# Kernel tuning notes

Hardware: AMD Instinct MI355X
Metric: run time of the kernel (lower is better)

## Reference

```python
import jax, jax.numpy as jnp
import numpy as np

FM = 256          # feature_maps
ROUNDS = 32
N_VARS = 4000
N_CLAUSES = 16800 # ~4.2 * n_vars (3-SAT phase transition)
K = 3             # literals per clause
EPS = 1e-8


def setup_inputs() -> dict:
    key = jax.random.key(0)
    ks = jax.random.split(key, 20)

    def nrm(k, shape):
        # tf.initializers.RandomNormal default stddev = 0.05
        return jax.random.normal(k, shape, jnp.float32) * 0.05

    vs = jax.random.randint(ks[0], (N_CLAUSES, K), 1, N_VARS + 1)
    sg = jnp.where(jax.random.uniform(ks[1], (N_CLAUSES, K)) < 0.5, -1, 1)
    return {
        "clause_lits": (vs * sg).astype(jnp.int32),  # signed 1-based literals
        "n_vars": N_VARS,
        "L_init": nrm(ks[2], (1, FM)), "C_init": nrm(ks[3], (1, FM)),
        "LC_W0": nrm(ks[4], (FM, FM)), "LC_b0": jnp.zeros((FM,), jnp.float32),
        "LC_W1": nrm(ks[5], (FM, FM)), "LC_b1": jnp.zeros((FM,), jnp.float32),
        "LC_W2": nrm(ks[6], (FM, FM)), "LC_b2": jnp.zeros((FM,), jnp.float32),
        "CL_W0": nrm(ks[7], (FM, FM)), "CL_b0": jnp.zeros((FM,), jnp.float32),
        "CL_W1": nrm(ks[8], (FM, FM)), "CL_b1": jnp.zeros((FM,), jnp.float32),
        "CL_W2": nrm(ks[9], (FM, FM)), "CL_b2": jnp.zeros((FM,), jnp.float32),
        "C_Wx": nrm(ks[10], (FM, 4 * FM)), "C_Wh": nrm(ks[11], (FM, 4 * FM)),
        "C_b": jnp.zeros((4 * FM,), jnp.float32),
        "L_Wx": nrm(ks[12], (2 * FM, 4 * FM)), "L_Wh": nrm(ks[13], (FM, 4 * FM)),
        "L_b": jnp.zeros((4 * FM,), jnp.float32),
        "V_W0": nrm(ks[14], (2 * FM, 2 * FM)), "V_b0": jnp.zeros((2 * FM,), jnp.float32),
        "V_W1": nrm(ks[15], (2 * FM, 2 * FM)), "V_b1": jnp.zeros((2 * FM,), jnp.float32),
        "V_W2": nrm(ks[16], (2 * FM, 1)), "V_b2": jnp.zeros((1,), jnp.float32),
    }


def _mlp3(x, W0, b0, W1, b1, W2, b2):
    h = jax.nn.relu(x @ W0 + b0)
    h = jax.nn.relu(h @ W1 + b1)
    return h @ W2 + b2


def _lstm(x, h, c, Wx, Wh, b):
    # keras LSTMCell: gate order i, f, g, o; sigmoid recurrent, tanh activation
    z = x @ Wx + h @ Wh + b
    i, f, g, o = jnp.split(z, 4, axis=1)
    c = jax.nn.sigmoid(f) * c + jax.nn.sigmoid(i) * jnp.tanh(g)
    h = jax.nn.sigmoid(o) * jnp.tanh(c)
    return h, c


def reference(clause_lits, n_vars, L_init, C_init,
              LC_W0, LC_b0, LC_W1, LC_b1, LC_W2, LC_b2,
              CL_W0, CL_b0, CL_W1, CL_b1, CL_W2, CL_b2,
              C_Wx, C_Wh, C_b, L_Wx, L_Wh, L_b,
              V_W0, V_b0, V_W1, V_b1, V_W2, V_b2):
    n_clauses = clause_lits.shape[0]
    n_lits = 2 * n_vars
    lits = clause_lits.reshape(-1)                         # [E]
    sign = jnp.sign(lits).astype(jnp.float32)              # [E]
    var_idx = jnp.abs(lits) - 1                            # [E] 0-based var
    lit_idx = jnp.where(lits > 0, var_idx, n_vars + var_idx)
    clause_idx = jnp.repeat(jnp.arange(n_clauses), clause_lits.shape[1])

    denom = jnp.sqrt(jnp.float32(FM))
    l_h = jnp.tile(L_init / denom, (n_lits, 1))
    c_h = jnp.tile(C_init / denom, (n_clauses, 1))
    l_c = jnp.zeros_like(l_h)
    c_c = jnp.zeros_like(c_h)

    def vote(lh):
        variables = jnp.concatenate([lh[:n_vars], lh[n_vars:]], axis=1)  # [n_vars, 2*FM]
        return _mlp3(variables, V_W0, V_b0, V_W1, V_b1, V_W2, V_b2)      # [n_vars, 1]

    def clause_loss(logits):
        # softplus_log_square_loss: clause_val = exp(-sum_lit softplus(sign*logit))
        vals = logits[var_idx, 0] * sign                   # [E]
        s = jax.ops.segment_sum(jax.nn.softplus(vals), clause_idx,
                                num_segments=n_clauses, indices_are_sorted=True)
        cv = jnp.exp(-s)
        return jnp.sum(jnp.square(-jnp.log(1.0 - cv + EPS)))

    def round_fn(carry, _):
        lh, lc, ch, cc, loss = carry
        lc_pre = _mlp3(lh, LC_W0, LC_b0, LC_W1, LC_b1, LC_W2, LC_b2)
        # SpMM adj^T @ msgs: scatter literal messages into clauses
        lc_msgs = jax.ops.segment_sum(lc_pre[lit_idx], clause_idx,
                                      num_segments=n_clauses, indices_are_sorted=True)
        ch, cc = _lstm(lc_msgs, ch, cc, C_Wx, C_Wh, C_b)
        cl_pre = _mlp3(ch, CL_W0, CL_b0, CL_W1, CL_b1, CL_W2, CL_b2)
        # SpMM adj @ msgs: scatter clause messages into literals
        cl_msgs = jax.ops.segment_sum(cl_pre[clause_idx], lit_idx, num_segments=n_lits)
        flipped = jnp.concatenate([lh[n_vars:], lh[:n_vars]], axis=0)
        lh, lc = _lstm(jnp.concatenate([cl_msgs, flipped], axis=1), lh, lc,
                       L_Wx, L_Wh, L_b)
        loss = loss + clause_loss(vote(lh))
        return (lh, lc, ch, cc, loss), None

    (l_h, l_c, c_h, c_c, loss), _ = jax.lax.scan(
        round_fn, (l_h, l_c, c_h, c_c, jnp.float32(0.0)), None, length=ROUNDS)
    logits = vote(l_h)
    return logits, loss / jnp.float32(ROUNDS)
```

## Files before the change

### kernel.cpp

```cpp
#include <hip/hip_runtime.h>
#include <hip/hip_bf16.h>

#define NV 4000
#define NL 8000
#define NC 16800
#define NE 50400
#define FM 256
#define ROUNDS 32

typedef short s16x8 __attribute__((ext_vector_type(8)));
typedef __bf16 b16x8 __attribute__((ext_vector_type(8)));
typedef float f32x4 __attribute__((ext_vector_type(4)));
union V8 { s16x8 s; b16x8 b; ushort u[8]; };

using gaddr_t = const void __attribute__((address_space(1)))*;
using laddr_t = void __attribute__((address_space(3)))*;

__device__ __forceinline__ float b2f(ushort u) {
    union { uint i; float f; } v; v.i = ((uint)u) << 16; return v.f;
}
__device__ __forceinline__ ushort f2b(float f) {
    __hip_bfloat16 h = __float2bfloat16(f);
    return *(ushort*)&h;
}

__global__ void zero_kernel(float* __restrict__ p, int n) {
    int i = blockIdx.x * blockDim.x + threadIdx.x;
    if (i < n) p[i] = 0.0f;
}
__global__ void f2b_kernel(const float* __restrict__ src, ushort* __restrict__ dst, int n) {
    int i = blockIdx.x * blockDim.x + threadIdx.x;
    if (i < n) dst[i] = f2b(src[i]);
}
__global__ void transpose_w_kernel(const float* __restrict__ in, ushort* __restrict__ out,
                                   int K, int N, int ldo, int koff, int perm) {
    int idx = blockIdx.x * blockDim.x + threadIdx.x;
    if (idx >= K * N) return;
    int n = idx / K, k = idx - n * K;
    int row = perm ? ((n & 255) * 4 + (n >> 8)) : n;
    out[(size_t)row * ldo + koff + k] = f2b(in[(size_t)k * N + n]);
}
__global__ void permute_bias_kernel(const float* __restrict__ b, float* __restrict__ bp) {
    int n = blockIdx.x * blockDim.x + threadIdx.x;
    if (n < 1024) bp[(n & 255) * 4 + (n >> 8)] = b[n];
}

__global__ void init_lh_kernel(const float* __restrict__ Li, ushort* __restrict__ lh) {
    int idx = blockIdx.x * blockDim.x + threadIdx.x;
    if (idx < NL * FM) lh[idx] = f2b(Li[idx & (FM - 1)] * (1.0f / 16.0f));
}
__global__ void init_ch_kernel(const float* __restrict__ Ci, ushort* __restrict__ ch) {
    int idx = blockIdx.x * blockDim.x + threadIdx.x;
    if (idx < NC * FM) ch[idx] = f2b(Ci[idx & (FM - 1)] * (1.0f / 16.0f));
}

__global__ void csr_count_kernel(const int* __restrict__ lits, int* __restrict__ deg) {
    int e = blockIdx.x * blockDim.x + threadIdx.x;
    if (e >= NE) return;
    int l = lits[e];
    int v = (l > 0 ? l : -l) - 1;
    int li = (l > 0) ? v : NV + v;
    atomicAdd(&deg[li], 1);
}
__global__ void csr_scan_kernel(const int* __restrict__ deg, int* __restrict__ rowptr,
                                int* __restrict__ nxt) {
    if (threadIdx.x == 0 && blockIdx.x == 0) {
        int acc = 0;
        for (int i = 0; i < NL; ++i) { rowptr[i] = acc; nxt[i] = acc; acc += deg[i]; }
        rowptr[NL] = acc;
    }
}
__global__ void csr_fill_kernel(const int* __restrict__ lits, int* __restrict__ nxt,
                                int* __restrict__ ecl) {
    int e = blockIdx.x * blockDim.x + threadIdx.x;
    if (e >= NE) return;
    int l = lits[e];
    int v = (l > 0 ? l : -l) - 1;
    int li = (l > 0) ? v : NV + v;
    int pos = atomicAdd(&nxt[li], 1);
    ecl[pos] = e / 3;
}

#define BKT 64

#define MLPR 32
__global__ __launch_bounds__(256) void mlp3_kernel(
    const ushort* __restrict__ A,
    const ushort* __restrict__ W0t, const float* __restrict__ b0,
    const ushort* __restrict__ W1t, const float* __restrict__ b1,
    const ushort* __restrict__ W2t, const float* __restrict__ b2,
    ushort* __restrict__ out, int M)
{
    __shared__ __align__(16) ushort As[MLPR * BKT];
    __shared__ __align__(16) ushort Wl[256 * BKT];
    __shared__ __align__(16) ushort Ab[MLPR * 264];
    const int tid = threadIdx.x;
    const int lane = tid & 63, wid = tid >> 6;
    const int rowBase = blockIdx.x * MLPR;
    const int lr = lane >> 3, ql = (lane & 7) ^ lr;
    const int cl16 = lane & 15, kg = lane >> 4;

    const ushort* Wt[3] = {W0t, W1t, W2t};
    const float*  bs[3] = {b0, b1, b2};

    #pragma unroll
    for (int layer = 0; layer < 3; ++layer) {
        f32x4 acc[2][4];
        #pragma unroll
        for (int i = 0; i < 2; ++i)
            #pragma unroll
            for (int j = 0; j < 4; ++j) acc[i][j] = (f32x4){0.f, 0.f, 0.f, 0.f};

        for (int kt = 0; kt < 4; ++kt) {
            __syncthreads();
            #pragma unroll
            for (int t = 0; t < 8; ++t) {
                int row = wid * 64 + t * 8 + lr;
                __builtin_amdgcn_global_load_lds(
                    (gaddr_t)(Wt[layer] + (size_t)row * 256 + kt * 64 + ql * 8),
                    (laddr_t)&Wl[(wid * 64 + t * 8) * BKT + lane * 8], 16, 0, 0);
            }
            if (layer == 0) {
                int row = rowBase + wid * 8 + lr;
                if (row > M - 1) row = M - 1;
                __builtin_amdgcn_global_load_lds(
                    (gaddr_t)(A + (size_t)row * 256 + kt * 64 + ql * 8),
                    (laddr_t)&As[wid * 512 + lane * 8], 16, 0, 0);
            }
            __syncthreads();
            #pragma unroll
            for (int s = 0; s < 2; ++s) {
                int kq8 = s * 4 + kg;
                V8 af[2], bf[4];
                #pragma unroll
                for (int i = 0; i < 2; ++i) {
                    int m = i * 16 + cl16;
                    if (layer == 0)
                        af[i].s = *(const s16x8*)&As[m * BKT + ((kq8 ^ (m & 7)) * 8)];
                    else
                        af[i].s = *(const s16x8*)&Ab[m * 264 + kt * 64 + kq8 * 8];
                }
                #pragma unroll
                for (int j = 0; j < 4; ++j) {
                    int n = wid * 64 + j * 16 + cl16;
                    bf[j].s = *(const s16x8*)&Wl[n * BKT + ((kq8 ^ (n & 7)) * 8)];
                }
                #pragma unroll
                for (int i = 0; i < 2; ++i)
                    #pragma unroll
                    for (int j = 0; j < 4; ++j)
                        acc[i][j] = __builtin_amdgcn_mfma_f32_16x16x32_bf16(
                            af[i].b, bf[j].b, acc[i][j], 0, 0, 0);
            }
        }
        __syncthreads();
        const int rq = (lane >> 4) * 4;
        #pragma unroll
        for (int i = 0; i < 2; ++i)
            #pragma unroll
            for (int r = 0; r < 4; ++r) {
                int row = i * 16 + rq + r;
                #pragma unroll
                for (int j = 0; j < 4; ++j) {
                    int col = wid * 64 + j * 16 + cl16;
                    float v = acc[i][j][r] + bs[layer][col];
                    if (layer < 2) {
                        Ab[row * 264 + col] = f2b(fmaxf(v, 0.0f));
                    } else {
                        int grow = rowBase + row;
                        if (grow < M) out[(size_t)grow * 256 + col] = f2b(v);
                    }
                }
            }
    }
}

__global__ __launch_bounds__(256) void gemm16_n64_kernel(
    const ushort* __restrict__ A0, int K0,
    const ushort* __restrict__ A1, int K1,
    const ushort* __restrict__ Bt, const float* __restrict__ bias,
    ushort* __restrict__ C, int M, int N, int relu)
{
    __shared__ __align__(16) ushort Al[128 * BKT];
    __shared__ __align__(16) ushort Bl[64 * BKT];
    const int Ktot = K0 + K1;
    const int tid = threadIdx.x;
    const int rowBase = blockIdx.y * 128, colBase = blockIdx.x * 64;
    const int lane = tid & 63, wid = tid >> 6;
    const int wm = (wid & 1) * 64, wn = (wid >> 1) * 32;
    const int lr = lane >> 3, ql = (lane & 7) ^ lr;

    f32x4 acc[4][2];
    #pragma unroll
    for (int i = 0; i < 4; ++i)
        #pragma unroll
        for (int j = 0; j < 2; ++j) acc[i][j] = (f32x4){0.f, 0.f, 0.f, 0.f};

    for (int k0 = 0; k0 < Ktot; k0 += BKT) {
        const ushort* As; int ks, lda;
        if (k0 < K0) { As = A0; ks = k0; lda = K0; }
        else         { As = A1; ks = k0 - K0; lda = K1; }
        __syncthreads();
        #pragma unroll
        for (int t = 0; t < 4; ++t) {
            int rloc = (wid * 4 + t) * 8 + lr;
            int ga = rowBase + rloc; if (ga > M - 1) ga = M - 1;
            __builtin_amdgcn_global_load_lds((gaddr_t)(As + (size_t)ga * lda + ks + ql * 8),
                                             (laddr_t)&Al[(wid * 4 + t) * 512], 16, 0, 0);
        }
        #pragma unroll
        for (int t = 0; t < 2; ++t) {
            int rloc = (wid * 2 + t) * 8 + lr;
            __builtin_amdgcn_global_load_lds((gaddr_t)(Bt + (size_t)(colBase + rloc) * Ktot + k0 + ql * 8),
                                             (laddr_t)&Bl[(wid * 2 + t) * 512], 16, 0, 0);
        }
        __syncthreads();
        const int cl = lane & 15, kg = lane >> 4;
        #pragma unroll
        for (int s = 0; s < 2; ++s) {
            V8 af[4], bf[2];
            #pragma unroll
            for (int i = 0; i < 4; ++i) {
                int m = wm + i * 16 + cl;
                af[i].s = *(const s16x8*)&Al[m * BKT + (((s * 4 + kg) ^ (m & 7)) * 8)];
            }
            #pragma unroll
            for (int j = 0; j < 2; ++j) {
                int n = wn + j * 16 + cl;
                bf[j].s = *(const s16x8*)&Bl[n * BKT + (((s * 4 + kg) ^ (n & 7)) * 8)];
            }
            #pragma unroll
            for (int i = 0; i < 4; ++i)
                #pragma unroll
                for (int j = 0; j < 2; ++j)
                    acc[i][j] = __builtin_amdgcn_mfma_f32_16x16x32_bf16(af[i].b, bf[j].b,
                                                                        acc[i][j], 0, 0, 0);
        }
    }
    const int rq = (lane >> 4) * 4, cl = lane & 15;
    #pragma unroll
    for (int i = 0; i < 4; ++i)
        #pragma unroll
        for (int r = 0; r < 4; ++r) {
            int grow = rowBase + wm + i * 16 + rq + r;
            if (grow >= M) continue;
            #pragma unroll
            for (int j = 0; j < 2; ++j) {
                int gcol = colBase + wn + j * 16 + cl;
                float v = acc[i][j][r] + bias[gcol];
                if (relu) v = fmaxf(v, 0.0f);
                C[(size_t)grow * N + gcol] = f2b(v);
            }
        }
}

__global__ __launch_bounds__(256) void gemm_lstm_kernel(
    const ushort* __restrict__ A0, int K0,
    const ushort* __restrict__ A1, int K1,
    const ushort* __restrict__ A2, int K2,
    int flip1,
    const ushort* __restrict__ Bt, const float* __restrict__ biasP,
    float* __restrict__ c32, ushort* __restrict__ h_out, int M)
{
    __shared__ __align__(16) ushort smem[2 * 128 * BKT];
    ushort* Al = smem;
    ushort* Bl = smem + 128 * BKT;
    const int Ktot = K0 + K1 + K2;
    const int tid = threadIdx.x;
    const int rowBase = blockIdx.y * 128, colBase = blockIdx.x * 128;
    const int lane = tid & 63, wid = tid >> 6;
    const int wm = (wid >> 1) * 64, wn = (wid & 1) * 64;
    const int lr = lane >> 3, ql = (lane & 7) ^ lr;

    f32x4 acc[4][4];
    #pragma unroll
    for (int i = 0; i < 4; ++i)
        #pragma unroll
        for (int j = 0; j < 4; ++j) acc[i][j] = (f32x4){0.f, 0.f, 0.f, 0.f};

    for (int k0 = 0; k0 < Ktot; k0 += BKT) {
        const ushort* As; int ks, lda, flip;
        if (k0 < K0)           { As = A0; ks = k0;           lda = K0; flip = 0; }
        else if (k0 < K0 + K1) { As = A1; ks = k0 - K0;      lda = K1; flip = flip1; }
        else                   { As = A2; ks = k0 - K0 - K1; lda = K2; flip = 0; }
        __syncthreads();
        #pragma unroll
        for (int t = 0; t < 4; ++t) {
            int rloc = (wid * 4 + t) * 8 + lr;
            int ga = rowBase + rloc; if (ga > M - 1) ga = M - 1;
            if (flip) ga = (ga < NV) ? ga + NV : ga - NV;
            __builtin_amdgcn_global_load_lds((gaddr_t)(As + (size_t)ga * lda + ks + ql * 8),
                                             (laddr_t)&Al[(wid * 4 + t) * 512], 16, 0, 0);
            __builtin_amdgcn_global_load_lds((gaddr_t)(Bt + (size_t)(colBase + rloc) * Ktot + k0 + ql * 8),
                                             (laddr_t)&Bl[(wid * 4 + t) * 512], 16, 0, 0);
        }
        __syncthreads();
        const int cl = lane & 15, kg = lane >> 4;
        #pragma unroll
        for (int s = 0; s < 2; ++s) {
            V8 af[4], bf[4];
            #pragma unroll
            for (int i = 0; i < 4; ++i) {
                int m = wm + i * 16 + cl;
                af[i].s = *(const s16x8*)&Al[m * BKT + (((s * 4 + kg) ^ (m & 7)) * 8)];
            }
            #pragma unroll
            for (int j = 0; j < 4; ++j) {
                int n = wn + j * 16 + cl;
                bf[j].s = *(const s16x8*)&Bl[n * BKT + (((s * 4 + kg) ^ (n & 7)) * 8)];
            }
            #pragma unroll
            for (int i = 0; i < 4; ++i)
                #pragma unroll
                for (int j = 0; j < 4; ++j)
                    acc[i][j] = __builtin_amdgcn_mfma_f32_16x16x32_bf16(af[i].b, bf[j].b,
                                                                        acc[i][j], 0, 0, 0);
        }
    }
    __syncthreads();
    {
        const int rq = (lane >> 4) * 4, cl = lane & 15;
        #pragma unroll
        for (int i = 0; i < 4; ++i)
            #pragma unroll
            for (int r = 0; r < 4; ++r) {
                int rl = wm + i * 16 + rq + r;
                #pragma unroll
                for (int j = 0; j < 4; ++j) {
                    int clc = wn + j * 16 + cl;
                    smem[rl * 128 + clc] = f2b(acc[i][j][r] + biasP[colBase + clc]);
                }
            }
    }
    __syncthreads();
    const int fl = tid & 31, rg = tid >> 5;
    const int fglob = (colBase >> 2) + fl;
    #pragma unroll
    for (int k = 0; k < 16; ++k) {
        int rl = rg + 8 * k;
        int grow = rowBase + rl;
        if (grow >= M) continue;
        ushort4 g4 = *(const ushort4*)&smem[rl * 128 + fl * 4];
        float zi = b2f(g4.x), zf = b2f(g4.y), zg = b2f(g4.z), zo = b2f(g4.w);
        size_t ci = (size_t)grow * FM + fglob;
        float cold = c32[ci];
        float si = 1.0f / (1.0f + __expf(-zi));
        float sf = 1.0f / (1.0f + __expf(-zf));
        float so = 1.0f / (1.0f + __expf(-zo));
        float cn = sf * cold + si * tanhf(zg);
        float hn = so * tanhf(cn);
        c32[ci] = cn;
        h_out[ci] = f2b(hn);
    }
}

__global__ void gather_lc8_kernel(const ushort* __restrict__ pre, const int* __restrict__ lits,
                                  ushort* __restrict__ out) {
    int idx = blockIdx.x * blockDim.x + threadIdx.x;
    if (idx >= NC * 32) return;
    int c = idx >> 5, f8 = (idx & 31) * 8;
    const int* cl = lits + c * 3;
    float s[8] = {};
    #pragma unroll
    for (int k = 0; k < 3; ++k) {
        int l = cl[k];
        int v = (l > 0 ? l : -l) - 1;
        int li = (l > 0) ? v : NV + v;
        V8 x; x.s = *(const s16x8*)&pre[(size_t)li * FM + f8];
        #pragma unroll
        for (int e = 0; e < 8; ++e) s[e] += b2f(x.u[e]);
    }
    V8 o;
    #pragma unroll
    for (int e = 0; e < 8; ++e) o.u[e] = f2b(s[e]);
    *(s16x8*)&out[(size_t)c * FM + f8] = o.s;
}

__global__ void gather_cl8_kernel(const ushort* __restrict__ pre, const int* __restrict__ rowptr,
                                  const int* __restrict__ ecl, ushort* __restrict__ out) {
    int idx = blockIdx.x * blockDim.x + threadIdx.x;
    if (idx >= NL * 32) return;
    int li = idx >> 5, f8 = (idx & 31) * 8;
    int j0 = rowptr[li], j1 = rowptr[li + 1];
    float s[8] = {};
    for (int j = j0; j < j1; ++j) {
        V8 x; x.s = *(const s16x8*)&pre[(size_t)ecl[j] * FM + f8];
        #pragma unroll
        for (int e = 0; e < 8; ++e) s[e] += b2f(x.u[e]);
    }
    V8 o;
    #pragma unroll
    for (int e = 0; e < 8; ++e) o.u[e] = f2b(s[e]);
    *(s16x8*)&out[(size_t)li * FM + f8] = o.s;
}

__global__ void vote_out_kernel(const ushort* __restrict__ h1, const ushort* __restrict__ w,
                                const float* __restrict__ b, float* __restrict__ logits_hist,
                                float* __restrict__ out_f32) {
    int gtid = blockIdx.x * blockDim.x + threadIdx.x;
    int wid = gtid >> 6;
    int lane = threadIdx.x & 63;
    if (wid >= NV) return;
    const ushort* hr = h1 + (size_t)wid * 512;
    float s = 0.0f;
    #pragma unroll
    for (int k = 0; k < 8; ++k) s += b2f(hr[lane + 64 * k]) * b2f(w[lane + 64 * k]);
    #pragma unroll
    for (int off = 32; off; off >>= 1) s += __shfl_down(s, off);
    if (lane == 0) {
        float v = s + b[0];
        logits_hist[wid] = v;
        if (out_f32) out_f32[wid] = v;
    }
}

__global__ __launch_bounds__(256) void loss_all_kernel(
    const float* __restrict__ logits_hist, const int* __restrict__ lits,
    float* __restrict__ loss_arr)
{
    __shared__ float sm[256];
    const int r = blockIdx.y;
    const float* logits = logits_hist + (size_t)r * NV;
    int c = blockIdx.x * 256 + threadIdx.x;
    float t2 = 0.0f;
    if (c < NC) {
        const int* cl = lits + c * 3;
        float s = 0.0f;
        #pragma unroll
        for (int k = 0; k < 3; ++k) {
            int l = cl[k];
            int v = (l > 0 ? l : -l) - 1;
            float sg = (l > 0) ? 1.0f : -1.0f;
            float val = logits[v] * sg;
            s += fmaxf(val, 0.0f) + log1pf(__expf(-fabsf(val)));
        }
        float cv = __expf(-s);
        float t = -logf(1.0f - cv + 1e-8f);
        t2 = t * t;
    }
    sm[threadIdx.x] = t2;
    __syncthreads();
    for (int st = 128; st > 0; st >>= 1) {
        if (threadIdx.x < st) sm[threadIdx.x] += sm[threadIdx.x + st];
        __syncthreads();
    }
    if (threadIdx.x == 0) atomicAdd(&loss_arr[r], sm[0]);
}

__global__ void final_loss_kernel(const float* __restrict__ loss_arr, float* __restrict__ out) {
    if (threadIdx.x == 0 && blockIdx.x == 0) {
        float s = 0.0f;
        for (int r = 0; r < ROUNDS; ++r) s += loss_arr[r];
        out[NV] = s * (1.0f / (float)ROUNDS);
    }
}

extern "C" void kernel_launch(void* const* d_in, const int* in_sizes, int n_in,
                              void* d_out, int out_size, void* d_ws, size_t ws_size,
                              hipStream_t stream) {
    const int* lits = (const int*)d_in[0];
    float* out = (float*)d_out;

    const float* Li   = (const float*)d_in[2];
    const float* Ci   = (const float*)d_in[3];
    const float* LCW0 = (const float*)d_in[4];
    const float* LCb0 = (const float*)d_in[5];
    const float* LCW1 = (const float*)d_in[6];
    const float* LCb1 = (const float*)d_in[7];
    const float* LCW2 = (const float*)d_in[8];
    const float* LCb2 = (const float*)d_in[9];
    const float* CLW0 = (const float*)d_in[10];
    const float* CLb0 = (const float*)d_in[11];
    const float* CLW1 = (const float*)d_in[12];
    const float* CLb1 = (const float*)d_in[13];
    const float* CLW2 = (const float*)d_in[14];
    const float* CLb2 = (const float*)d_in[15];
    const float* CWx  = (const float*)d_in[16];
    const float* CWh  = (const float*)d_in[17];
    const float* Cb   = (const float*)d_in[18];
    const float* LWx  = (const float*)d_in[19];
    const float* LWh  = (const float*)d_in[20];
    const float* Lb   = (const float*)d_in[21];
    const float* VW0  = (const float*)d_in[22];
    const float* Vb0  = (const float*)d_in[23];
    const float* VW1  = (const float*)d_in[24];
    const float* Vb1  = (const float*)d_in[25];
    const float* VW2  = (const float*)d_in[26];
    const float* Vb2  = (const float*)d_in[27];
    (void)in_sizes; (void)n_in; (void)out_size; (void)ws_size;

    char* base = (char*)d_ws;
    size_t off = 0;
    auto allocB = [&](size_t bytes) {
        void* p = base + off;
        off += (bytes + 15) & ~(size_t)15;
        return p;
    };
    float*  loss_arr    = (float*)allocB(ROUNDS * 4);
    float*  logits_hist = (float*)allocB((size_t)ROUNDS * NV * 4);
    float*  lc32        = (float*)allocB((size_t)NL * FM * 4);
    float*  cc32        = (float*)allocB((size_t)NC * FM * 4);
    float*  Cb_p        = (float*)allocB(1024 * 4);
    float*  Lb_p        = (float*)allocB(1024 * 4);
    int*    deg         = (int*)allocB(NL * 4);
    int*    rowptr      = (int*)allocB((NL + 1) * 4);
    int*    nxt         = (int*)allocB(NL * 4);
    int*    ecl         = (int*)allocB(NE * 4);
    ushort* LC0t = (ushort*)allocB((size_t)256 * 256 * 2);
    ushort* LC1t = (ushort*)allocB((size_t)256 * 256 * 2);
    ushort* LC2t = (ushort*)allocB((size_t)256 * 256 * 2);
    ushort* CL0t = (ushort*)allocB((size_t)256 * 256 * 2);
    ushort* CL1t = (ushort*)allocB((size_t)256 * 256 * 2);
    ushort* CL2t = (ushort*)allocB((size_t)256 * 256 * 2);
    ushort* CWt  = (ushort*)allocB((size_t)1024 * 512 * 2);
    ushort* LWt  = (ushort*)allocB((size_t)1024 * 768 * 2);
    ushort* VW0t = (ushort*)allocB((size_t)512 * 512 * 2);
    ushort* VW1t = (ushort*)allocB((size_t)512 * 512 * 2);
    ushort* vw2  = (ushort*)allocB((size_t)512 * 2);
    ushort* lh_a = (ushort*)allocB((size_t)NL * FM * 2);
    ushort* lh_b = (ushort*)allocB((size_t)NL * FM * 2);
    ushort* ch_a = (ushort*)allocB((size_t)NC * FM * 2);
    ushort* ch_b = (ushort*)allocB((size_t)NC * FM * 2);
    ushort* lcm16 = (ushort*)allocB((size_t)NC * FM * 2);
    ushort* clm16 = (ushort*)allocB((size_t)NL * FM * 2);
    ushort* tL    = (ushort*)allocB((size_t)NL * FM * 2);
    ushort* tC    = (ushort*)allocB((size_t)NC * FM * 2);
    ushort* v0    = (ushort*)allocB((size_t)NV * 512 * 2);
    ushort* v1    = (ushort*)allocB((size_t)NV * 512 * 2);

    auto tw = [&](const float* in, ushort* o, int K, int N, int ldo, int koff, int perm) {
        hipLaunchKernelGGL(transpose_w_kernel, dim3((K * N + 255) / 256), dim3(256), 0, stream,
                           in, o, K, N, ldo, koff, perm);
    };
    tw(LCW0, LC0t, 256, 256, 256, 0, 0);
    tw(LCW1, LC1t, 256, 256, 256, 0, 0);
    tw(LCW2, LC2t, 256, 256, 256, 0, 0);
    tw(CLW0, CL0t, 256, 256, 256, 0, 0);
    tw(CLW1, CL1t, 256, 256, 256, 0, 0);
    tw(CLW2, CL2t, 256, 256, 256, 0, 0);
    tw(CWx,  CWt, 256, 1024, 512, 0, 1);
    tw(CWh,  CWt, 256, 1024, 512, 256, 1);
    tw(LWx,  LWt, 512, 1024, 768, 0, 1);
    tw(LWh,  LWt, 256, 1024, 768, 512, 1);
    tw(VW0,  VW0t, 512, 512, 512, 0, 0);
    tw(VW1,  VW1t, 512, 512, 512, 0, 0);
    hipLaunchKernelGGL(f2b_kernel, dim3(2), dim3(256), 0, stream, VW2, vw2, 512);
    hipLaunchKernelGGL(permute_bias_kernel, dim3(4), dim3(256), 0, stream, Cb, Cb_p);
    hipLaunchKernelGGL(permute_bias_kernel, dim3(4), dim3(256), 0, stream, Lb, Lb_p);

    hipLaunchKernelGGL(init_lh_kernel, dim3(NL * FM / 256), dim3(256), 0, stream, Li, lh_a);
    hipLaunchKernelGGL(init_ch_kernel, dim3(NC * FM / 256), dim3(256), 0, stream, Ci, ch_a);
    hipLaunchKernelGGL(zero_kernel, dim3(NL * FM / 256), dim3(256), 0, stream, lc32, NL * FM);
    hipLaunchKernelGGL(zero_kernel, dim3(NC * FM / 256), dim3(256), 0, stream, cc32, NC * FM);
    hipLaunchKernelGGL(zero_kernel, dim3(1), dim3(256), 0, stream, loss_arr, ROUNDS);
    hipLaunchKernelGGL(zero_kernel, dim3((NL + 255) / 256), dim3(256), 0, stream, (float*)deg, NL);
    hipLaunchKernelGGL(csr_count_kernel, dim3((NE + 255) / 256), dim3(256), 0, stream, lits, deg);
    hipLaunchKernelGGL(csr_scan_kernel, dim3(1), dim3(64), 0, stream, deg, rowptr, nxt);
    hipLaunchKernelGGL(csr_fill_kernel, dim3((NE + 255) / 256), dim3(256), 0, stream, lits, nxt, ecl);

    auto gemm64 = [&](const ushort* A0, int K0, const ushort* A1, int K1,
                      const ushort* Bt, const float* bias, ushort* C, int M, int N, int relu) {
        hipLaunchKernelGGL(gemm16_n64_kernel, dim3(N / 64, (M + 127) / 128), dim3(256), 0, stream,
                           A0, K0, A1, K1, Bt, bias, C, M, N, relu);
    };

    ushort *lh_c = lh_a, *lh_n = lh_b, *ch_c = ch_a, *ch_n = ch_b;

    for (int r = 0; r < ROUNDS; ++r) {
        hipLaunchKernelGGL(mlp3_kernel, dim3(NL / MLPR), dim3(256), 0, stream,
                           lh_c, LC0t, LCb0, LC1t, LCb1, LC2t, LCb2, tL, NL);
        hipLaunchKernelGGL(gather_lc8_kernel, dim3(NC * 32 / 256), dim3(256), 0, stream,
                           tL, lits, lcm16);
        hipLaunchKernelGGL(gemm_lstm_kernel, dim3(8, (NC + 127) / 128), dim3(256), 0, stream,
                           lcm16, 256, ch_c, 256, (const ushort*)0, 0, 0,
                           CWt, Cb_p, cc32, ch_n, NC);
        hipLaunchKernelGGL(mlp3_kernel, dim3(NC / MLPR, 1), dim3(256), 0, stream,
                           ch_n, CL0t, CLb0, CL1t, CLb1, CL2t, CLb2, tC, NC);
        hipLaunchKernelGGL(gather_cl8_kernel, dim3(NL * 32 / 256), dim3(256), 0, stream,
                           tC, rowptr, ecl, clm16);
        hipLaunchKernelGGL(gemm_lstm_kernel, dim3(8, (NL + 127) / 128), dim3(256), 0, stream,
                           clm16, 256, lh_c, 256, lh_c, 256, 1,
                           LWt, Lb_p, lc32, lh_n, NL);
        gemm64(lh_n, 256, lh_n + (size_t)NV * FM, 256, VW0t, Vb0, v0, NV, 512, 1);
        gemm64(v0, 512, 0, 0, VW1t, Vb1, v1, NV, 512, 1);
        hipLaunchKernelGGL(vote_out_kernel, dim3(NV * 64 / 256), dim3(256), 0, stream,
                           v1, vw2, Vb2, logits_hist + (size_t)r * NV,
                           (r == ROUNDS - 1) ? out : (float*)0);
        ushort* tswap;
        tswap = lh_c; lh_c = lh_n; lh_n = tswap;
        tswap = ch_c; ch_c = ch_n; ch_n = tswap;
    }

    hipLaunchKernelGGL(loss_all_kernel, dim3((NC + 255) / 256, ROUNDS), dim3(256), 0, stream,
                       logits_hist, lits, loss_arr);
    hipLaunchKernelGGL(final_loss_kernel, dim3(1), dim3(64), 0, stream, loss_arr, out);
}
```

Measured before the change: 5.726 ms.

## Fuse vote head into GEMM epilogue, parallelize CSR scan, merge setup kernels

The second vote-MLP GEMM now finishes the final 512->1 projection in its epilogue. It reduces across lanes with shuffles and adds into logits that are pre-filled with the output bias, using atomics. This removes the v1 buffer, its write and re-read, and one launch per round. Separately, the single-thread CSR prefix scan becomes a 1024-thread block scan, the six square weight transposes are batched into one launch, and the init and zero kernels are merged. The atomic accumulation makes the logit sums order-nondeterministic.

New measurement: 5.397 ms (median of 3 runs). -5.8%, faster.

```diff
diff --git a/kernel.cpp b/kernel.cpp
--- a/kernel.cpp
+++ b/kernel.cpp
@@ -31,6 +31,20 @@
 __global__ void f2b_kernel(const float* __restrict__ src, ushort* __restrict__ dst, int n) {
     int i = blockIdx.x * blockDim.x + threadIdx.x;
     if (i < n) dst[i] = f2b(src[i]);
+}
+__global__ void transpose_w6_kernel(
+    const float* __restrict__ s0, const float* __restrict__ s1, const float* __restrict__ s2,
+    const float* __restrict__ s3, const float* __restrict__ s4, const float* __restrict__ s5,
+    ushort* __restrict__ d0, ushort* __restrict__ d1, ushort* __restrict__ d2,
+    ushort* __restrict__ d3, ushort* __restrict__ d4, ushort* __restrict__ d5)
+{
+    const float* srcs[6] = {s0, s1, s2, s3, s4, s5};
+    ushort* dsts[6] = {d0, d1, d2, d3, d4, d5};
+    const float* in = srcs[blockIdx.y];
+    ushort* out = dsts[blockIdx.y];
+    int idx = blockIdx.x * blockDim.x + threadIdx.x;
+    int n = idx >> 8, k = idx & 255;
+    out[n * 256 + k] = f2b(in[k * 256 + n]);
 }
 __global__ void transpose_w_kernel(const float* __restrict__ in, ushort* __restrict__ out,
                                    int K, int N, int ldo, int koff, int perm) {
@@ -45,13 +59,18 @@
     if (n < 1024) bp[(n & 255) * 4 + (n >> 8)] = b[n];
 }
 
-__global__ void init_lh_kernel(const float* __restrict__ Li, ushort* __restrict__ lh) {
+__global__ void init_all_kernel(const float* __restrict__ Li, const float* __restrict__ Ci,
+                                ushort* __restrict__ lh, float* __restrict__ lc32,
+                                ushort* __restrict__ ch, float* __restrict__ cc32) {
     int idx = blockIdx.x * blockDim.x + threadIdx.x;
-    if (idx < NL * FM) lh[idx] = f2b(Li[idx & (FM - 1)] * (1.0f / 16.0f));
-}
-__global__ void init_ch_kernel(const float* __restrict__ Ci, ushort* __restrict__ ch) {
-    int idx = blockIdx.x * blockDim.x + threadIdx.x;
-    if (idx < NC * FM) ch[idx] = f2b(Ci[idx & (FM - 1)] * (1.0f / 16.0f));
+    if (idx < NL * FM) { lh[idx] = f2b(Li[idx & 255] * (1.0f / 16.0f)); lc32[idx] = 0.0f; }
+    if (idx < NC * FM) { ch[idx] = f2b(Ci[idx & 255] * (1.0f / 16.0f)); cc32[idx] = 0.0f; }
+}
+__global__ void fill_hist_kernel(float* __restrict__ hist, const float* __restrict__ b2,
+                                 float* __restrict__ loss_arr) {
+    int i = blockIdx.x * blockDim.x + threadIdx.x;
+    if (i < ROUNDS * NV) hist[i] = b2[0];
+    if (i < ROUNDS) loss_arr[i] = 0.0f;
 }
 
 __global__ void csr_count_kernel(const int* __restrict__ lits, int* __restrict__ deg) {
@@ -62,13 +81,36 @@
     int li = (l > 0) ? v : NV + v;
     atomicAdd(&deg[li], 1);
 }
-__global__ void csr_scan_kernel(const int* __restrict__ deg, int* __restrict__ rowptr,
-                                int* __restrict__ nxt) {
-    if (threadIdx.x == 0 && blockIdx.x == 0) {
-        int acc = 0;
-        for (int i = 0; i < NL; ++i) { rowptr[i] = acc; nxt[i] = acc; acc += deg[i]; }
-        rowptr[NL] = acc;
-    }
+__global__ __launch_bounds__(1024) void csr_scan_kernel(const int* __restrict__ deg,
+                                                        int* __restrict__ rowptr,
+                                                        int* __restrict__ nxt) {
+    __shared__ int ls[1024];
+    int t = threadIdx.x;
+    int base = t * 8;
+    int local[8];
+    int s = 0;
+    #pragma unroll
+    for (int i = 0; i < 8; ++i) {
+        int idx = base + i;
+        int d = (idx < NL) ? deg[idx] : 0;
+        local[i] = s;
+        s += d;
+    }
+    ls[t] = s;
+    __syncthreads();
+    for (int st = 1; st < 1024; st <<= 1) {
+        int v = (t >= st) ? ls[t - st] : 0;
+        __syncthreads();
+        ls[t] += v;
+        __syncthreads();
+    }
+    int prefix = (t == 0) ? 0 : ls[t - 1];
+    #pragma unroll
+    for (int i = 0; i < 8; ++i) {
+        int idx = base + i;
+        if (idx < NL) { int v = prefix + local[i]; rowptr[idx] = v; nxt[idx] = v; }
+    }
+    if (t == 1023) rowptr[NL] = ls[1023];
 }
 __global__ void csr_fill_kernel(const int* __restrict__ lits, int* __restrict__ nxt,
                                 int* __restrict__ ecl) {
@@ -251,6 +293,87 @@
                 if (relu) v = fmaxf(v, 0.0f);
                 C[(size_t)grow * N + gcol] = f2b(v);
             }
+        }
+}
+
+__global__ __launch_bounds__(256) void gemm16_vote_kernel(
+    const ushort* __restrict__ A0,
+    const ushort* __restrict__ Bt,
+    const float* __restrict__ bias,
+    const ushort* __restrict__ w2,
+    float* __restrict__ logits, int M)
+{
+    __shared__ __align__(16) ushort Al[128 * BKT];
+    __shared__ __align__(16) ushort Bl[64 * BKT];
+    const int Ktot = 512;
+    const int tid = threadIdx.x;
+    const int rowBase = blockIdx.y * 128, colBase = blockIdx.x * 64;
+    const int lane = tid & 63, wid = tid >> 6;
+    const int wm = (wid & 1) * 64, wn = (wid >> 1) * 32;
+    const int lr = lane >> 3, ql = (lane & 7) ^ lr;
+
+    f32x4 acc[4][2];
+    #pragma unroll
+    for (int i = 0; i < 4; ++i)
+        #pragma unroll
+        for (int j = 0; j < 2; ++j) acc[i][j] = (f32x4){0.f, 0.f, 0.f, 0.f};
+
+    for (int k0 = 0; k0 < Ktot; k0 += BKT) {
+        __syncthreads();
+        #pragma unroll
+        for (int t = 0; t < 4; ++t) {
+            int rloc = (wid * 4 + t) * 8 + lr;
+            int ga = rowBase + rloc; if (ga > M - 1) ga = M - 1;
+            __builtin_amdgcn_global_load_lds((gaddr_t)(A0 + (size_t)ga * Ktot + k0 + ql * 8),
+                                             (laddr_t)&Al[(wid * 4 + t) * 512], 16, 0, 0);
+        }
+        #pragma unroll
+        for (int t = 0; t < 2; ++t) {
+            int rloc = (wid * 2 + t) * 8 + lr;
+            __builtin_amdgcn_global_load_lds((gaddr_t)(Bt + (size_t)(colBase + rloc) * Ktot + k0 + ql * 8),
+                                             (laddr_t)&Bl[(wid * 2 + t) * 512], 16, 0, 0);
+        }
+        __syncthreads();
+        const int cl = lane & 15, kg = lane >> 4;
+        #pragma unroll
+        for (int s = 0; s < 2; ++s) {
+            V8 af[4], bf[2];
+            #pragma unroll
+            for (int i = 0; i < 4; ++i) {
+                int m = wm + i * 16 + cl;
+                af[i].s = *(const s16x8*)&Al[m * BKT + (((s * 4 + kg) ^ (m & 7)) * 8)];
+            }
+            #pragma unroll
+            for (int j = 0; j < 2; ++j) {
+                int n = wn + j * 16 + cl;
+                bf[j].s = *(const s16x8*)&Bl[n * BKT + (((s * 4 + kg) ^ (n & 7)) * 8)];
+            }
+            #pragma unroll
+            for (int i = 0; i < 4; ++i)
+                #pragma unroll
+                for (int j = 0; j < 2; ++j)
+                    acc[i][j] = __builtin_amdgcn_mfma_f32_16x16x32_bf16(af[i].b, bf[j].b,
+                                                                        acc[i][j], 0, 0, 0);
+        }
+    }
+    const int rq = (lane >> 4) * 4, cl = lane & 15;
+    #pragma unroll
+    for (int i = 0; i < 4; ++i)
+        #pragma unroll
+        for (int r = 0; r < 4; ++r) {
+            int grow = rowBase + wm + i * 16 + rq + r;
+            float s = 0.0f;
+            #pragma unroll
+            for (int j = 0; j < 2; ++j) {
+                int gcol = colBase + wn + j * 16 + cl;
+                float h1 = b2f(f2b(fmaxf(acc[i][j][r] + bias[gcol], 0.0f)));
+                s += h1 * b2f(w2[gcol]);
+            }
+            s += __shfl_xor(s, 1);
+            s += __shfl_xor(s, 2);
+            s += __shfl_xor(s, 4);
+            s += __shfl_xor(s, 8);
+            if (cl == 0 && grow < M) atomicAdd(&logits[grow], s);
         }
 }
 
@@ -394,26 +517,6 @@
     *(s16x8*)&out[(size_t)li * FM + f8] = o.s;
 }
 
-__global__ void vote_out_kernel(const ushort* __restrict__ h1, const ushort* __restrict__ w,
-                                const float* __restrict__ b, float* __restrict__ logits_hist,
-                                float* __restrict__ out_f32) {
-    int gtid = blockIdx.x * blockDim.x + threadIdx.x;
-    int wid = gtid >> 6;
-    int lane = threadIdx.x & 63;
-    if (wid >= NV) return;
-    const ushort* hr = h1 + (size_t)wid * 512;
-    float s = 0.0f;
-    #pragma unroll
-    for (int k = 0; k < 8; ++k) s += b2f(hr[lane + 64 * k]) * b2f(w[lane + 64 * k]);
-    #pragma unroll
-    for (int off = 32; off; off >>= 1) s += __shfl_down(s, off);
-    if (lane == 0) {
-        float v = s + b[0];
-        logits_hist[wid] = v;
-        if (out_f32) out_f32[wid] = v;
-    }
-}
-
 __global__ __launch_bounds__(256) void loss_all_kernel(
     const float* __restrict__ logits_hist, const int* __restrict__ lits,
     float* __restrict__ loss_arr)
@@ -447,8 +550,12 @@
     if (threadIdx.x == 0) atomicAdd(&loss_arr[r], sm[0]);
 }
 
-__global__ void final_loss_kernel(const float* __restrict__ loss_arr, float* __restrict__ out) {
-    if (threadIdx.x == 0 && blockIdx.x == 0) {
+__global__ void final_out_kernel(const float* __restrict__ logits_hist,
+                                 const float* __restrict__ loss_arr,
+                                 float* __restrict__ out) {
+    int i = blockIdx.x * blockDim.x + threadIdx.x;
+    if (i < NV) out[i] = logits_hist[(size_t)(ROUNDS - 1) * NV + i];
+    if (i == NV) {
         float s = 0.0f;
         for (int r = 0; r < ROUNDS; ++r) s += loss_arr[r];
         out[NV] = s * (1.0f / (float)ROUNDS);
@@ -526,18 +633,14 @@
     ushort* tL    = (ushort*)allocB((size_t)NL * FM * 2);
     ushort* tC    = (ushort*)allocB((size_t)NC * FM * 2);
     ushort* v0    = (ushort*)allocB((size_t)NV * 512 * 2);
-    ushort* v1    = (ushort*)allocB((size_t)NV * 512 * 2);
-
+
+    hipLaunchKernelGGL(transpose_w6_kernel, dim3(256, 6), dim3(256), 0, stream,
+                       LCW0, LCW1, LCW2, CLW0, CLW1, CLW2,
+                       LC0t, LC1t, LC2t, CL0t, CL1t, CL2t);
     auto tw = [&](const float* in, ushort* o, int K, int N, int ldo, int koff, int perm) {
         hipLaunchKernelGGL(transpose_w_kernel, dim3((K * N + 255) / 256), dim3(256), 0, stream,
                            in, o, K, N, ldo, koff, perm);
     };
-    tw(LCW0, LC0t, 256, 256, 256, 0, 0);
-    tw(LCW1, LC1t, 256, 256, 256, 0, 0);
-    tw(LCW2, LC2t, 256, 256, 256, 0, 0);
-    tw(CLW0, CL0t, 256, 256, 256, 0, 0);
-    tw(CLW1, CL1t, 256, 256, 256, 0, 0);
-    tw(CLW2, CL2t, 256, 256, 256, 0, 0);
     tw(CWx,  CWt, 256, 1024, 512, 0, 1);
     tw(CWh,  CWt, 256, 1024, 512, 256, 1);
     tw(LWx,  LWt, 512, 1024, 768, 0, 1);
@@ -547,22 +650,14 @@
     hipLaunchKernelGGL(f2b_kernel, dim3(2), dim3(256), 0, stream, VW2, vw2, 512);
     hipLaunchKernelGGL(permute_bias_kernel, dim3(4), dim3(256), 0, stream, Cb, Cb_p);
     hipLaunchKernelGGL(permute_bias_kernel, dim3(4), dim3(256), 0, stream, Lb, Lb_p);
-
-    hipLaunchKernelGGL(init_lh_kernel, dim3(NL * FM / 256), dim3(256), 0, stream, Li, lh_a);
-    hipLaunchKernelGGL(init_ch_kernel, dim3(NC * FM / 256), dim3(256), 0, stream, Ci, ch_a);
-    hipLaunchKernelGGL(zero_kernel, dim3(NL * FM / 256), dim3(256), 0, stream, lc32, NL * FM);
-    hipLaunchKernelGGL(zero_kernel, dim3(NC * FM / 256), dim3(256), 0, stream, cc32, NC * FM);
-    hipLaunchKernelGGL(zero_kernel, dim3(1), dim3(256), 0, stream, loss_arr, ROUNDS);
+    hipLaunchKernelGGL(init_all_kernel, dim3(NC * FM / 256), dim3(256), 0, stream,
+                       Li, Ci, lh_a, lc32, ch_a, cc32);
+    hipLaunchKernelGGL(fill_hist_kernel, dim3((ROUNDS * NV + 255) / 256), dim3(256), 0, stream,
+                       logits_hist, Vb2, loss_arr);
     hipLaunchKernelGGL(zero_kernel, dim3((NL + 255) / 256), dim3(256), 0, stream, (float*)deg, NL);
     hipLaunchKernelGGL(csr_count_kernel, dim3((NE + 255) / 256), dim3(256), 0, stream, lits, deg);
-    hipLaunchKernelGGL(csr_scan_kernel, dim3(1), dim3(64), 0, stream, deg, rowptr, nxt);
+    hipLaunchKernelGGL(csr_scan_kernel, dim3(1), dim3(1024), 0, stream, deg, rowptr, nxt);
     hipLaunchKernelGGL(csr_fill_kernel, dim3((NE + 255) / 256), dim3(256), 0, stream, lits, nxt, ecl);
-
-    auto gemm64 = [&](const ushort* A0, int K0, const ushort* A1, int K1,
-                      const ushort* Bt, const float* bias, ushort* C, int M, int N, int relu) {
-        hipLaunchKernelGGL(gemm16_n64_kernel, dim3(N / 64, (M + 127) / 128), dim3(256), 0, stream,
-                           A0, K0, A1, K1, Bt, bias, C, M, N, relu);
-    };
 
     ushort *lh_c = lh_a, *lh_n = lh_b, *ch_c = ch_a, *ch_n = ch_b;
 
@@ -581,11 +676,10 @@
         hipLaunchKernelGGL(gemm_lstm_kernel, dim3(8, (NL + 127) / 128), dim3(256), 0, stream,
                            clm16, 256, lh_c, 256, lh_c, 256, 1,
                            LWt, Lb_p, lc32, lh_n, NL);
-        gemm64(lh_n, 256, lh_n + (size_t)NV * FM, 256, VW0t, Vb0, v0, NV, 512, 1);
-        gemm64(v0, 512, 0, 0, VW1t, Vb1, v1, NV, 512, 1);
-        hipLaunchKernelGGL(vote_out_kernel, dim3(NV * 64 / 256), dim3(256), 0, stream,
-                           v1, vw2, Vb2, logits_hist + (size_t)r * NV,
-                           (r == ROUNDS - 1) ? out : (float*)0);
+        hipLaunchKernelGGL(gemm16_n64_kernel, dim3(8, (NV + 127) / 128), dim3(256), 0, stream,
+                           lh_n, 256, lh_n + (size_t)NV * FM, 256, VW0t, Vb0, v0, NV, 512, 1);
+        hipLaunchKernelGGL(gemm16_vote_kernel, dim3(8, (NV + 127) / 128), dim3(256), 0, stream,
+                           v0, VW1t, Vb1, vw2, logits_hist + (size_t)r * NV, NV);
         ushort* tswap;
         tswap = lh_c; lh_c = lh_n; lh_n = tswap;
         tswap = ch_c; ch_c = ch_n; ch_n = tswap;
@@ -593,5 +687,6 @@
 
     hipLaunchKernelGGL(loss_all_kernel, dim3((NC + 255) / 256, ROUNDS), dim3(256), 0, stream,
                        logits_hist, lits, loss_arr);
-    hipLaunchKernelGGL(final_loss_kernel, dim3(1), dim3(64), 0, stream, loss_arr, out);
-}
+    hipLaunchKernelGGL(final_out_kernel, dim3((NV + 256) / 256), dim3(256), 0, stream,
+                       logits_hist, loss_arr, out);
+}
```
